# Optimization experiments

Hardware: AMD Instinct MI355X
Metric: run time of the kernel (lower is better)

The kernel has to match this reference:

```python
import jax, jax.numpy as jnp
import numpy as np

PAD = 2  # F.conv2d(padding=2) with 5x5 kernels -> SAME

def setup_inputs() -> dict:
    key = jax.random.key(0)
    k1, k2 = jax.random.split(key)
    B, H, W, C = 64, 128, 128, 3
    KH, KW, N = 5, 5, 10  # last_frames(2) * num_transformed_images(5)
    images = jax.random.uniform(k1, (B, H, W, C), dtype=jnp.float32)
    kernels = jax.random.uniform(k2, (B, KH, KW, N), dtype=jnp.float32)
    return {"images": images, "kernels": kernels}


def reference(images, kernels):
    """Faithful JAX version of apply_cdna_kernels.

    images:  [B, H, W, C]
    kernels: [B, KH, KW, N]
    returns: [N, B, C, H, W] (the torch code returns N split tensors of
             shape [1, B, C, H, W]; we return the equivalent stacked array).
    Implemented as a single grouped cross-correlation with
    feature_group_count=B, fusing the per-batch F.conv2d loop.
    """
    B, H, W, C = images.shape
    _, KH, KW, N = kernels.shape
    # torch: images.permute([3,0,1,2]) -> [C, B, H, W]; treat C as conv batch,
    # B as input channels, one input channel per group.
    inp = jnp.transpose(images, (3, 0, 1, 2))  # [C, B, H, W]
    # weights: group b owns output channels b*N:(b+1)*N, each 1 input channel
    w = jnp.transpose(kernels, (0, 3, 1, 2)).reshape(B * N, 1, KH, KW)
    out = jax.lax.conv_general_dilated(
        inp, w,
        window_strides=(1, 1),
        padding=((PAD, PAD), (PAD, PAD)),
        feature_group_count=B,
        dimension_numbers=("NCHW", "OIHW", "NCHW"),
    )  # [C, B*N, H, W]
    out = out.reshape(C, B, N, H, W)
    return jnp.transpose(out, (2, 1, 0, 3, 4))  # [N, B, C, H, W]
```

## Files before the change

### kernel.cpp

```cpp
#include <hip/hip_runtime.h>


#define B_  64
#define H_  128
#define W_  128
#define C_  3
#define N_  10
#define KH_ 5
#define KW_ 5
#define TH_ 8
#define TW_ 32
#define HALO 2
#define LDS_ROW ((TW_ + 2*HALO) * C_)
#define LDS_ELEMS ((TH_ + 2*HALO) * LDS_ROW)

__global__ __launch_bounds__(256, 4) void cdna_apply_kernel(
    const float* __restrict__ images,
    const float* __restrict__ kernels,
    float* __restrict__ out)
{
    __shared__ float s_img[LDS_ELEMS];

    const int tid = threadIdx.x;
    const int bid = blockIdx.x;
    const int b   = bid >> 6;
    const int t   = bid & 63;
    const int by  = t >> 2;
    const int bx  = t & 3;
    const int y0  = by * TH_;
    const int x0  = bx * TW_;

    const long img_base = (long)b * (H_ * W_ * C_);
    #pragma unroll
    for (int i = tid; i < LDS_ELEMS; i += 256) {
        int yy = i / LDS_ROW;
        int r  = i - yy * LDS_ROW;
        int xx = r / C_;
        int c  = r - xx * C_;
        int y  = y0 + yy - HALO;
        int x  = x0 + xx - HALO;
        float v = 0.0f;
        if ((unsigned)y < (unsigned)H_ && (unsigned)x < (unsigned)W_)
            v = images[img_base + (long)y * (W_ * C_) + x * C_ + c];
        s_img[i] = v;
    }
    __syncthreads();

    const int tx = tid & (TW_ - 1);
    const int ty = tid >> 5;

    const float* __restrict__ kb = kernels + b * (KH_ * KW_ * N_);

    float acc[N_ * C_];
    #pragma unroll
    for (int i = 0; i < N_ * C_; ++i) acc[i] = 0.0f;

    #pragma unroll 1
    for (int kh = 0; kh < KH_; ++kh) {
        const float* row = &s_img[(ty + kh) * LDS_ROW + tx * C_];
        float p[KW_ * C_];
        #pragma unroll
        for (int i = 0; i < KW_ * C_; ++i) p[i] = row[i];

        const float* __restrict__ wrow = kb + kh * (KW_ * N_);
        #pragma unroll
        for (int kw = 0; kw < KW_; ++kw) {
            #pragma unroll
            for (int n = 0; n < N_; ++n) {
                const float wgt = wrow[kw * N_ + n];
                acc[n * C_ + 0] = fmaf(p[kw * C_ + 0], wgt, acc[n * C_ + 0]);
                acc[n * C_ + 1] = fmaf(p[kw * C_ + 1], wgt, acc[n * C_ + 1]);
                acc[n * C_ + 2] = fmaf(p[kw * C_ + 2], wgt, acc[n * C_ + 2]);
            }
        }
    }

    const int h = y0 + ty;
    const int w = x0 + tx;
    float* ob = out + (long)b * (C_ * H_ * W_) + (long)h * W_ + w;
    #pragma unroll
    for (int n = 0; n < N_; ++n) {
        #pragma unroll
        for (int c = 0; c < C_; ++c) {
            ob[(long)n * ((long)B_ * C_ * H_ * W_) + (long)c * (H_ * W_)] = acc[n * C_ + c];
        }
    }
}

extern "C" void kernel_launch(void* const* d_in, const int* in_sizes, int n_in,
                              void* d_out, int out_size, void* d_ws, size_t ws_size,
                              hipStream_t stream) {
    const float* images  = (const float*)d_in[0];
    const float* kernels = (const float*)d_in[1];
    float* out = (float*)d_out;

    const int grid = B_ * (H_ / TH_) * (W_ / TW_);
    cdna_apply_kernel<<<grid, 256, 0, stream>>>(images, kernels, out);
}
```

Before: 149.0 us.

## Compute two adjacent output pixels per thread with wider tiles and float2 stores

After: 153.1 us. +2.7%, slower.

```diff
diff --git a/kernel.cpp b/kernel.cpp
--- a/kernel.cpp
+++ b/kernel.cpp
@@ -9,9 +9,9 @@
 #define KH_ 5
 #define KW_ 5
 #define TH_ 8
-#define TW_ 32
+#define TWB 64
 #define HALO 2
-#define LDS_ROW ((TW_ + 2*HALO) * C_)
+#define LDS_ROW ((TWB + 2*HALO) * C_)
 #define LDS_ELEMS ((TH_ + 2*HALO) * LDS_ROW)
 
 __global__ __launch_bounds__(256, 4) void cdna_apply_kernel(
@@ -23,44 +23,47 @@
 
     const int tid = threadIdx.x;
     const int bid = blockIdx.x;
-    const int b   = bid >> 6;
-    const int t   = bid & 63;
-    const int by  = t >> 2;
-    const int bx  = t & 3;
+    const int b   = bid >> 5;
+    const int t   = bid & 31;
+    const int by  = t >> 1;
+    const int bx  = t & 1;
     const int y0  = by * TH_;
-    const int x0  = bx * TW_;
+    const int x0  = bx * TWB;
 
     const long img_base = (long)b * (H_ * W_ * C_);
+    const int  colf0    = x0 * C_ - HALO * C_;
     #pragma unroll
-    for (int i = tid; i < LDS_ELEMS; i += 256) {
-        int yy = i / LDS_ROW;
-        int r  = i - yy * LDS_ROW;
-        int xx = r / C_;
-        int c  = r - xx * C_;
-        int y  = y0 + yy - HALO;
-        int x  = x0 + xx - HALO;
-        float v = 0.0f;
-        if ((unsigned)y < (unsigned)H_ && (unsigned)x < (unsigned)W_)
-            v = images[img_base + (long)y * (W_ * C_) + x * C_ + c];
-        s_img[i] = v;
+    for (int k = 0; k < (LDS_ELEMS + 255) / 256; ++k) {
+        int i = tid + k * 256;
+        if (i < LDS_ELEMS) {
+            int yy = i / LDS_ROW;
+            int r  = i - yy * LDS_ROW;
+            int y  = y0 + yy - HALO;
+            int cf = colf0 + r;
+            float v = 0.0f;
+            if ((unsigned)y < (unsigned)H_ && (unsigned)cf < (unsigned)(W_ * C_))
+                v = images[img_base + (long)y * (W_ * C_) + cf];
+            s_img[i] = v;
+        }
     }
     __syncthreads();
 
-    const int tx = tid & (TW_ - 1);
+    const int tx = tid & 31;
     const int ty = tid >> 5;
 
     const float* __restrict__ kb = kernels + b * (KH_ * KW_ * N_);
 
-    float acc[N_ * C_];
+    float acc0[N_ * C_];
+    float acc1[N_ * C_];
     #pragma unroll
-    for (int i = 0; i < N_ * C_; ++i) acc[i] = 0.0f;
+    for (int i = 0; i < N_ * C_; ++i) { acc0[i] = 0.0f; acc1[i] = 0.0f; }
 
     #pragma unroll 1
     for (int kh = 0; kh < KH_; ++kh) {
-        const float* row = &s_img[(ty + kh) * LDS_ROW + tx * C_];
-        float p[KW_ * C_];
+        const float* row = &s_img[(ty + kh) * LDS_ROW + 6 * tx];
+        float p[(KW_ + 1) * C_];
         #pragma unroll
-        for (int i = 0; i < KW_ * C_; ++i) p[i] = row[i];
+        for (int i = 0; i < (KW_ + 1) * C_; ++i) p[i] = row[i];
 
         const float* __restrict__ wrow = kb + kh * (KW_ * N_);
         #pragma unroll
@@ -68,21 +71,26 @@
             #pragma unroll
             for (int n = 0; n < N_; ++n) {
                 const float wgt = wrow[kw * N_ + n];
-                acc[n * C_ + 0] = fmaf(p[kw * C_ + 0], wgt, acc[n * C_ + 0]);
-                acc[n * C_ + 1] = fmaf(p[kw * C_ + 1], wgt, acc[n * C_ + 1]);
-                acc[n * C_ + 2] = fmaf(p[kw * C_ + 2], wgt, acc[n * C_ + 2]);
+                #pragma unroll
+                for (int c = 0; c < C_; ++c) {
+                    acc0[n * C_ + c] = fmaf(p[kw * C_ + c],       wgt, acc0[n * C_ + c]);
+                    acc1[n * C_ + c] = fmaf(p[kw * C_ + C_ + c],  wgt, acc1[n * C_ + c]);
+                }
             }
         }
     }
 
     const int h = y0 + ty;
-    const int w = x0 + tx;
+    const int w = x0 + 2 * tx;
     float* ob = out + (long)b * (C_ * H_ * W_) + (long)h * W_ + w;
     #pragma unroll
     for (int n = 0; n < N_; ++n) {
         #pragma unroll
         for (int c = 0; c < C_; ++c) {
-            ob[(long)n * ((long)B_ * C_ * H_ * W_) + (long)c * (H_ * W_)] = acc[n * C_ + c];
+            float2 v;
+            v.x = acc0[n * C_ + c];
+            v.y = acc1[n * C_ + c];
+            *(float2*)(ob + (long)n * ((long)B_ * C_ * H_ * W_) + (long)c * (H_ * W_)) = v;
         }
     }
 }
@@ -94,6 +102,6 @@
     const float* kernels = (const float*)d_in[1];
     float* out = (float*)d_out;
 
-    const int grid = B_ * (H_ / TH_) * (W_ / TW_);
+    const int grid = B_ * (H_ / TH_) * (W_ / TWB);
     cdna_apply_kernel<<<grid, 256, 0, stream>>>(images, kernels, out);
 }
```
